# Kernel tuning notes

Measured on AMD Instinct MI355X. Metric: run time of the kernel, lower is better.

## Reference

```python
import jax, jax.numpy as jnp
import numpy as np

B, C, H, W = 64, 1, 256, 256        # x shape; seq_len = C*H = 256, input_dim = W = 256
E, HID, L, NCLS = 512, 1024, 2, 10


def _lstm_layer(xs, h0, c0, Wx, bx, Wh, bh):
    """xs: [S,B,in] -> ys: [S,B,HID]. Gate order: f, i, g(candidate), o."""
    def step(carry, xt):
        h, c = carry
        gates = xt @ Wx + bx + h @ Wh + bh            # [B, 4*HID] (fuses 8 tiny Linears into 2 GEMMs)
        f, i, g, o = jnp.split(gates, 4, axis=-1)
        f = jax.nn.sigmoid(f)
        i = jax.nn.sigmoid(i)
        g = jnp.tanh(g)
        o = jax.nn.sigmoid(o)
        c = f * c + i * g
        h = o * jnp.tanh(c)
        return (h, c), h
    (hT, cT), ys = jax.lax.scan(step, (h0, c0), xs)
    return ys


def setup_inputs() -> dict:
    key = jax.random.key(0)
    ks = jax.random.split(key, 16)
    s = 0.02
    inp = {
        "x": jax.random.normal(ks[0], (B, C, H, W), jnp.float32),
        "h0": jax.random.normal(ks[1], (L, B, HID), jnp.float32),
        "c0": jax.random.normal(ks[2], (L, B, HID), jnp.float32),
        "W_enc": jax.random.normal(ks[3], (W, E), jnp.float32) * s,
        "b_enc": jnp.zeros((E,), jnp.float32),
        "alpha": jnp.float32(0.25),  # PReLU default single-parameter weight
        "Wx0": jax.random.normal(ks[4], (E, 4 * HID), jnp.float32) * s,
        "bx0": jnp.zeros((4 * HID,), jnp.float32),
        "Wh0": jax.random.normal(ks[5], (HID, 4 * HID), jnp.float32) * s,
        "bh0": jnp.zeros((4 * HID,), jnp.float32),
        "Wx1": jax.random.normal(ks[6], (HID, 4 * HID), jnp.float32) * s,
        "bx1": jnp.zeros((4 * HID,), jnp.float32),
        "Wh1": jax.random.normal(ks[7], (HID, 4 * HID), jnp.float32) * s,
        "bh1": jnp.zeros((4 * HID,), jnp.float32),
        "W_cls": jax.random.normal(ks[8], (HID, NCLS), jnp.float32) * s,
        "b_cls": jnp.zeros((NCLS,), jnp.float32),
    }
    return inp


def reference(x, h0, c0, W_enc, b_enc, alpha, Wx0, bx0, Wh0, bh0,
              Wx1, bx1, Wh1, bh1, W_cls, b_cls):
    b, c, h, w = x.shape
    x = x.reshape(b, c * h, w)                    # [B, S, input_dim]
    e = x @ W_enc + b_enc                         # encoder Linear
    e = jnp.where(e >= 0, e, alpha * e)           # PReLU (single shared alpha)
    xs = jnp.swapaxes(e, 0, 1)                    # [S, B, E] for scan
    ys = _lstm_layer(xs, h0[0], c0[0], Wx0, bx0, Wh0, bh0)
    ys = _lstm_layer(ys, h0[1], c0[1], Wx1, bx1, Wh1, bh1)
    return ys[-1] @ W_cls + b_cls                 # classify last timestep -> [B, 10]
```

## Files before the change

kernel.cpp:

```cpp
#include <hip/hip_runtime.h>
#include <hip/hip_bf16.h>
#include <cstddef>


using short8 = __attribute__((ext_vector_type(8))) short;
using f32x4  = __attribute__((ext_vector_type(4))) float;

#define LD8(p) (*reinterpret_cast<const short8*>(p))

__device__ __forceinline__ float sigmoidf_(float x) {
    return 1.f / (1.f + __expf(-x));
}
__device__ __forceinline__ unsigned short f2bf(float x) {
    union { float f; unsigned u; } v; v.f = x;
    unsigned r = v.u + 0x7fffu + ((v.u >> 16) & 1u);
    return (unsigned short)(r >> 16);
}
__device__ __forceinline__ float bf2f(unsigned short h) {
    union { unsigned u; float f; } v; v.u = ((unsigned)h) << 16;
    return v.f;
}

__global__ __launch_bounds__(256) void xsplit_k(
    const float* __restrict__ x, unsigned short* __restrict__ Xhi,
    unsigned short* __restrict__ Xlo)
{
    const int idx = blockIdx.x * 256 + threadIdx.x;
    const int m = idx >> 5, kq = idx & 31;
    const int b = m & 63, t = m >> 6;
    const float* src = x + (size_t)b * 65536 + (size_t)t * 256 + kq * 8;
    short8 hv, lv;
#pragma unroll
    for (int e = 0; e < 8; ++e) {
        const float f = src[e];
        const unsigned short h = f2bf(f);
        hv[e] = (short)h;
        lv[e] = (short)f2bf(f - bf2f(h));
    }
    const size_t o = (size_t)m * 256 + kq * 8;
    *reinterpret_cast<short8*>(Xhi + o) = hv;
    *reinterpret_cast<short8*>(Xlo + o) = lv;
}

__global__ __launch_bounds__(256) void bsplitN_k(
    const float* __restrict__ W, unsigned short* __restrict__ Bhi,
    unsigned short* __restrict__ Blo, int K, int N)
{
    __shared__ float tl[32][65];
    const int k0 = blockIdx.x * 32, n0 = blockIdx.y * 64;
    const int tid = threadIdx.x;
    {
        const int kk = tid >> 3, nq = tid & 7;
#pragma unroll
        for (int j = 0; j < 2; ++j) {
            const float4 v = *reinterpret_cast<const float4*>(
                &W[(size_t)(k0 + kk) * N + n0 + nq * 8 + j * 4]);
            tl[kk][nq * 8 + j * 4 + 0] = v.x; tl[kk][nq * 8 + j * 4 + 1] = v.y;
            tl[kk][nq * 8 + j * 4 + 2] = v.z; tl[kk][nq * 8 + j * 4 + 3] = v.w;
        }
    }
    __syncthreads();
    const int n = tid >> 2, kq = tid & 3;
    short8 hv, lv;
#pragma unroll
    for (int j = 0; j < 8; ++j) {
        const float xv = tl[kq * 8 + j][n];
        const unsigned short h = f2bf(xv);
        hv[j] = (short)h;
        lv[j] = (short)f2bf(xv - bf2f(h));
    }
    const size_t o = (size_t)(n0 + n) * K + k0 + kq * 8;
    *reinterpret_cast<short8*>(&Bhi[o]) = hv;
    *reinterpret_cast<short8*>(&Blo[o]) = lv;
}

__global__ __launch_bounds__(256) void enc_mfma_k(
    const unsigned short* __restrict__ Ahi, const unsigned short* __restrict__ Alo,
    const unsigned short* __restrict__ Bhi, const unsigned short* __restrict__ Blo,
    unsigned short* __restrict__ Ef, const float* __restrict__ benc,
    const float* __restrict__ alphap)
{
    __shared__ float smemf[10240];
    unsigned short* const smemh = (unsigned short*)smemf;
    unsigned short* const As0 = smemh;
    unsigned short* const As1 = smemh + 5120;
    unsigned short* const Bs0 = smemh + 10240;
    unsigned short* const Bs1 = smemh + 15360;

    const int tid = threadIdx.x;
    const int lane = tid & 63, wid = tid >> 6;
    const int wm = wid >> 1, wn = wid & 1;
    const int m0 = blockIdx.y * 128;
    const int n0 = blockIdx.x * 128;
    const int K = 256;

    f32x4 acc[4][4] = {};

    const int sr = tid & 127;
    const int spl = tid >> 7;
    const unsigned short* Ag = (spl ? Alo : Ahi) + (size_t)(m0 + sr) * K;
    const unsigned short* Bg = (spl ? Blo : Bhi) + (size_t)(n0 + sr) * K;
    unsigned short* Asw = (spl ? As1 : As0) + sr * 40;
    unsigned short* Bsw = (spl ? Bs1 : Bs0) + sr * 40;
    const int sw = sr & 3;

    const int kg = lane >> 4;
    const int fr = lane & 15;

    for (int k0 = 0; k0 < K; k0 += 32) {
        short8 av[4], bv[4];
#pragma unroll
        for (int c = 0; c < 4; ++c) {
            av[c] = LD8(Ag + k0 + c * 8);
            bv[c] = LD8(Bg + k0 + c * 8);
        }
        __syncthreads();
#pragma unroll
        for (int c = 0; c < 4; ++c) {
            *reinterpret_cast<short8*>(Asw + ((c ^ sw) * 8)) = av[c];
            *reinterpret_cast<short8*>(Bsw + ((c ^ sw) * 8)) = bv[c];
        }
        __syncthreads();

        short8 af[2][4], bf[2][4];
#pragma unroll
        for (int i = 0; i < 4; ++i) {
            const int ra = wm * 64 + i * 16 + fr;
            const int rb = wn * 64 + i * 16 + fr;
            af[0][i] = LD8(As0 + ra * 40 + ((kg ^ (ra & 3)) * 8));
            af[1][i] = LD8(As1 + ra * 40 + ((kg ^ (ra & 3)) * 8));
            bf[0][i] = LD8(Bs0 + rb * 40 + ((kg ^ (rb & 3)) * 8));
            bf[1][i] = LD8(Bs1 + rb * 40 + ((kg ^ (rb & 3)) * 8));
        }
#pragma unroll
        for (int i = 0; i < 4; ++i)
#pragma unroll
            for (int j = 0; j < 4; ++j) {
                acc[i][j] = __builtin_amdgcn_mfma_f32_16x16x32_bf16(
                    af[0][i], bf[0][j], acc[i][j], 0, 0, 0);
                acc[i][j] = __builtin_amdgcn_mfma_f32_16x16x32_bf16(
                    af[0][i], bf[1][j], acc[i][j], 0, 0, 0);
                acc[i][j] = __builtin_amdgcn_mfma_f32_16x16x32_bf16(
                    af[1][i], bf[0][j], acc[i][j], 0, 0, 0);
            }
    }
    __syncthreads();

    float* slab = smemf + wid * 1040;
    const int t = (m0 >> 6) + wm;
    const int fq = lane >> 4;
    const float alpha = alphap[0];
#pragma unroll 1
    for (int j = 0; j < 4; ++j) {
#pragma unroll
        for (int i = 0; i < 4; ++i)
#pragma unroll
            for (int rr = 0; rr < 4; ++rr)
                slab[fr * 65 + i * 16 + fq * 4 + rr] = acc[i][j][rr];
        __syncthreads();
        const int b = lane;
        const int nj = b >> 4;
#pragma unroll
        for (int ng = 0; ng < 4; ++ng) {
            const int n = n0 + wn * 64 + j * 16 + ng * 4;
            unsigned short hs[4], ls[4];
#pragma unroll
            for (int v = 0; v < 4; ++v) {
                float f = slab[(ng * 4 + v) * 65 + b] + benc[n + v];
                f = (f >= 0.f) ? f : alpha * f;
                hs[v] = f2bf(f);
                ls[v] = f2bf(f - bf2f(hs[v]));
            }
            uint2 hp, lp;
            hp.x = (unsigned)hs[0] | ((unsigned)hs[1] << 16);
            hp.y = (unsigned)hs[2] | ((unsigned)hs[3] << 16);
            lp.x = (unsigned)ls[0] | ((unsigned)ls[1] << 16);
            lp.y = (unsigned)ls[2] | ((unsigned)ls[3] << 16);
            const int s = n >> 5, kgn = (n >> 3) & 3, e0 = n & 7;
            const int ln = (b & 15) + 16 * kgn;
            const size_t base =
                ((((size_t)t * 32 + s) * 4 + nj) * 64 + ln) * 8 + e0;
            *reinterpret_cast<uint2*>(Ef + base) = hp;
            *reinterpret_cast<uint2*>(Ef + base + 32768) = lp;
        }
        __syncthreads();
    }
}

__global__ __launch_bounds__(256) void wprep_k(
    const float* __restrict__ Wa, const float* __restrict__ Wb,
    unsigned short* __restrict__ Wf, int NS)
{
    __shared__ float tl[32][65];
    const int k0 = blockIdx.x * 32, j0 = blockIdx.y * 64;
    const int tid = threadIdx.x;
    {
        const int kk = tid >> 3, jq = tid & 7;
        const int k = k0 + kk;
        const float* src = (k < 1024) ? &Wa[(size_t)k * 4096]
                                      : &Wb[(size_t)(k - 1024) * 4096];
#pragma unroll
        for (int h = 0; h < 2; ++h) {
            const float4 v = *reinterpret_cast<const float4*>(
                &src[j0 + jq * 8 + h * 4]);
            tl[kk][jq * 8 + h * 4 + 0] = v.x; tl[kk][jq * 8 + h * 4 + 1] = v.y;
            tl[kk][jq * 8 + h * 4 + 2] = v.z; tl[kk][jq * 8 + h * 4 + 3] = v.w;
        }
    }
    __syncthreads();
    const int j = tid >> 2, kg = tid & 3;
    const int jg = j0 + j;
    const int g = jg >> 10, cc = jg & 1023;
    const int lb = cc >> 3, c = cc & 7;
    const int rloc = g * 8 + c;
    const int mi = rloc >> 4, r16 = rloc & 15;
    const int lane = r16 + 16 * kg;
    const int s = k0 >> 5;
    short8 hv, lv;
#pragma unroll
    for (int e = 0; e < 8; ++e) {
        const float x = tl[kg * 8 + e][j];
        const unsigned short h = f2bf(x);
        hv[e] = (short)h;
        lv[e] = (short)f2bf(x - bf2f(h));
    }
    const size_t oH = ((((size_t)lb * 2 + 0) * NS + s) * 2 + mi) * 512 + (size_t)lane * 8;
    const size_t oL = ((((size_t)lb * 2 + 1) * NS + s) * 2 + mi) * 512 + (size_t)lane * 8;
    *reinterpret_cast<short8*>(Wf + oH) = hv;
    *reinterpret_cast<short8*>(Wf + oL) = lv;
}

__global__ __launch_bounds__(256) void hsplit_k(
    const float* __restrict__ hrow, unsigned short* __restrict__ dst)
{
    const int idx = blockIdx.x * 256 + threadIdx.x;
    const int b = idx >> 7, gc = idx & 127;
    const int k = gc * 8;
    short8 hv, lv;
#pragma unroll
    for (int e = 0; e < 8; ++e) {
        const float x = hrow[(size_t)b * 1024 + k + e];
        const unsigned short h = f2bf(x);
        hv[e] = (short)h;
        lv[e] = (short)f2bf(x - bf2f(h));
    }
    const int s = k >> 5, kg = (k >> 3) & 3, nj = b >> 4;
    const int l = (b & 15) + 16 * kg;
    const size_t oH = (((size_t)(0 * 32 + s) * 4 + nj) * 64 + l) * 8;
    const size_t oL = (((size_t)(1 * 32 + s) * 4 + nj) * 64 + l) * 8;
    *reinterpret_cast<short8*>(dst + oH) = hv;
    *reinterpret_cast<short8*>(dst + oL) = lv;
}

__global__ __launch_bounds__(256) void bsum_k(
    const float* __restrict__ bx, const float* __restrict__ bh,
    float* __restrict__ out)
{
    const int r = blockIdx.x * 256 + threadIdx.x;
    const int lb = r >> 5, rl = r & 31;
    const int g = rl >> 3, c = rl & 7;
    const int j = g * 1024 + lb * 8 + c;
    out[r] = bx[j] + bh[j];
}

__global__ __launch_bounds__(512, 2) void fused_lstm_k(
    const unsigned short* __restrict__ Ef,
    const unsigned short* __restrict__ Wf0,
    const unsigned short* __restrict__ Wf1,
    unsigned short* __restrict__ Y0, unsigned short* __restrict__ H1,
    const float* __restrict__ c0, const float* __restrict__ bsum0p,
    const float* __restrict__ bsum1p, float* __restrict__ hst1,
    unsigned* bar)
{
    __shared__ float Pred[8][32][66];
    __shared__ unsigned short hasmH[64][8];
    __shared__ unsigned short hasmL[64][8];

    const int tid = threadIdx.x;
    const int lane = tid & 63;
    const int w = tid >> 6;
    const int bid = blockIdx.x;
    const int layer = bid >> 7;
    const int lb = bid & 127;

    const int NS = layer ? 64 : 48;
    const int nEx = layer ? 4 : 2;
    const int wNS = NS * 1024;

    const unsigned short* Wf = layer ? Wf1 : Wf0;
    const unsigned short* wB =
        Wf + (size_t)lb * 2 * NS * 1024 + (size_t)lane * 8;

    short8 w00r[8], w01r[8], w10r[8], w11r[8];
#pragma unroll
    for (int i = 0; i < 8; ++i)
        if (i < 4 + nEx) {
            const int sg = (i < 4)
                ? (w * 4 + i)
                : (layer ? (32 + w * 4 + (i - 4)) : (32 + w * 2 + (i - 4)));
            const unsigned short* wp = wB + (size_t)sg * 1024;
            w00r[i] = LD8(wp);        w01r[i] = LD8(wp + 512);
            w10r[i] = LD8(wp + wNS);  w11r[i] = LD8(wp + wNS + 512);
        }

    const int col = w;
    float c_ = c0[(size_t)layer * 65536 + (size_t)lane * 1024 + lb * 8 + col];
    const float* bsB = layer ? bsum1p : bsum0p;
    float bs[4];
#pragma unroll
    for (int g = 0; g < 4; ++g) bs[g] = bsB[lb * 32 + g * 8 + col];

#define MM(mi, nj, HH, HL)                                                     \
    acc[mi][nj] = __builtin_amdgcn_mfma_f32_16x16x32_bf16(                     \
        (mi) ? w01r[i] : w00r[i], HH, acc[mi][nj], 0, 0, 0);                   \
    acc[mi][nj] = __builtin_amdgcn_mfma_f32_16x16x32_bf16(                     \
        (mi) ? w01r[i] : w00r[i], HL, acc[mi][nj], 0, 0, 0);                   \
    acc[mi][nj] = __builtin_amdgcn_mfma_f32_16x16x32_bf16(                     \
        (mi) ? w11r[i] : w10r[i], HH, acc[mi][nj], 0, 0, 0);
#define SUBTILE(hp, po)                                                        \
    {                                                                          \
        const short8 h0v = LD8(hp),        h1v = LD8(hp + 512);                \
        const short8 h2v = LD8(hp + 1024), h3v = LD8(hp + 1536);               \
        const short8 l0v = LD8(hp + po),        l1v = LD8(hp + po + 512);      \
        const short8 l2v = LD8(hp + po + 1024), l3v = LD8(hp + po + 1536);     \
        MM(0, 0, h0v, l0v)  MM(0, 1, h1v, l1v)                                 \
        MM(0, 2, h2v, l2v)  MM(0, 3, h3v, l3v)                                 \
        MM(1, 0, h0v, l0v)  MM(1, 1, h1v, l1v)                                 \
        MM(1, 2, h2v, l2v)  MM(1, 3, h3v, l3v)                                 \
    }
#define WPOLL(baseIdx, need)                                                   \
    {                                                                          \
        if (lane < 16) {                                                       \
            unsigned* p = bar + (size_t)((baseIdx) + lane) * 32;               \
            while (__hip_atomic_load(p, __ATOMIC_RELAXED,                      \
                                     __HIP_MEMORY_SCOPE_AGENT) < (need))       \
                __builtin_amdgcn_s_sleep(1);                                   \
        }                                                                      \
        __builtin_amdgcn_wave_barrier();                                       \
        asm volatile("" ::: "memory");                                         \
    }

    for (int r = 1; r <= 257; ++r) {
        const bool act = layer ? (r >= 2) : (r <= 256);
        if (act) {
            const int t = layer ? r - 2 : r - 1;
            const unsigned short* hOwn =
                (layer ? H1 : Y0) + (size_t)t * 131072 + (size_t)lane * 8;
            const unsigned short* hCross = layer
                ? Y0 + (size_t)(t + 1) * 131072 + (size_t)lane * 8
                : Ef + (size_t)t * 65536 + (size_t)lane * 8;
            const int poCross = layer ? 65536 : 32768;

            f32x4 acc[2][4] = {};

            if (layer) WPOLL(w * 16, (unsigned)(r - 1))
#pragma unroll
            for (int i = 4; i < 8; ++i)
                if (i < 4 + nEx) {
                    const int cs = layer ? (w * 4 + (i - 4)) : (w * 2 + (i - 4));
                    const unsigned short* hp = hCross + (size_t)cs * 2048;
                    SUBTILE(hp, poCross)
                }

            if (r >= 2) WPOLL((layer ? 128 : 0) + w * 16, (unsigned)(r - 1))
#pragma unroll
            for (int i = 0; i < 4; ++i) {
                const unsigned short* hp = hOwn + (size_t)(w * 4 + i) * 2048;
                SUBTILE(hp, 65536)
            }

            {
                const int rq = (lane >> 4) * 4, cq = lane & 15;
#pragma unroll
                for (int mi = 0; mi < 2; ++mi)
#pragma unroll
                    for (int nj = 0; nj < 4; ++nj)
#pragma unroll
                        for (int rr = 0; rr < 4; ++rr)
                            Pred[w][mi * 16 + rq + rr][nj * 16 + cq] =
                                acc[mi][nj][rr];
            }
            __syncthreads();

            {
                float p[4];
#pragma unroll
                for (int g = 0; g < 4; ++g) {
                    const int row = g * 8 + col;
                    float s0 = 0.f;
#pragma unroll
                    for (int ww = 0; ww < 8; ++ww)
                        s0 += Pred[ww][row][lane];
                    p[g] = s0 + bs[g];
                }
                const float fg = sigmoidf_(p[0]);
                const float ig = sigmoidf_(p[1]);
                const float gg = tanhf(p[2]);
                const float og = sigmoidf_(p[3]);
                c_ = fmaf(fg, c_, ig * gg);
                const float h = og * tanhf(c_);
                const unsigned short hh = f2bf(h);
                hasmH[lane][col] = hh;
                hasmL[lane][col] = f2bf(h - bf2f(hh));
                if (layer && r == 257)
                    hst1[(size_t)(lb * 8 + col) * 64 + lane] = h;
            }
            __syncthreads();

            if (tid < 128) {
                const int p = tid >> 6, b = tid & 63;
                unsigned short* hw =
                    (layer ? H1 : Y0) + (size_t)(t + 1) * 131072;
                const size_t off =
                    (((size_t)(p * 32 + (lb >> 2)) * 4 + (b >> 4)) * 64 +
                     ((b & 15) + 16 * (lb & 3))) * 8;
                const unsigned long long* src =
                    reinterpret_cast<const unsigned long long*>(
                        p ? &hasmL[b][0] : &hasmH[b][0]);
                unsigned long long* dst =
                    reinterpret_cast<unsigned long long*>(hw + off);
                __hip_atomic_store(dst, src[0], __ATOMIC_RELAXED,
                                   __HIP_MEMORY_SCOPE_AGENT);
                __hip_atomic_store(dst + 1, src[1], __ATOMIC_RELAXED,
                                   __HIP_MEMORY_SCOPE_AGENT);
            }
        }

        if (r <= 256) {
            __syncthreads();
            if (tid == 0)
                __hip_atomic_store(bar + (size_t)bid * 32, (unsigned)r,
                                   __ATOMIC_RELAXED, __HIP_MEMORY_SCOPE_AGENT);
        }
    }
#undef WPOLL
#undef SUBTILE
#undef MM
}

__global__ __launch_bounds__(256) void cls_k(
    const float* __restrict__ hfin, const float* __restrict__ Wc,
    const float* __restrict__ bcls, float* __restrict__ out)
{
    __shared__ float red[4][64];
    const int n = blockIdx.x;
    const int lane = threadIdx.x & 63, w = threadIdx.x >> 6;
    float acc = 0.f;
    for (int k = w * 256; k < w * 256 + 256; ++k)
        acc = fmaf(hfin[k * 64 + lane], Wc[k * 10 + n], acc);
    red[w][lane] = acc;
    __syncthreads();
    if (w == 0) {
        out[lane * 10 + n] = red[0][lane] + red[1][lane] + red[2][lane] +
                             red[3][lane] + bcls[n];
    }
}

extern "C" void kernel_launch(void* const* d_in, const int* in_sizes, int n_in,
                              void* d_out, int out_size, void* d_ws,
                              size_t ws_size, hipStream_t stream)
{
    const float* x    = (const float*)d_in[0];
    const float* h0   = (const float*)d_in[1];
    const float* c0   = (const float*)d_in[2];
    const float* Wenc = (const float*)d_in[3];
    const float* benc = (const float*)d_in[4];
    const float* alpha= (const float*)d_in[5];
    const float* Wx0  = (const float*)d_in[6];
    const float* bx0  = (const float*)d_in[7];
    const float* Wh0  = (const float*)d_in[8];
    const float* bh0  = (const float*)d_in[9];
    const float* Wx1  = (const float*)d_in[10];
    const float* bx1  = (const float*)d_in[11];
    const float* Wh1  = (const float*)d_in[12];
    const float* bh1  = (const float*)d_in[13];
    const float* Wcls = (const float*)d_in[14];
    const float* bcls = (const float*)d_in[15];
    float* out = (float*)d_out;

    float* ws = (float*)d_ws;
    size_t off = 0;
    unsigned short* Ef   = (unsigned short*)(ws + off); off += 8388608;
    unsigned short* Wf0  = (unsigned short*)(ws + off); off += 6291456;
    unsigned short* Wf1  = (unsigned short*)(ws + off); off += 8388608;
    unsigned short* Y0   = (unsigned short*)(ws + off); off += 16842752;
    unsigned short* H1   = (unsigned short*)(ws + off); off += 16842752;
    unsigned short* Xhi  = (unsigned short*)(ws + off); off += 2097152;
    unsigned short* Xlo  = (unsigned short*)(ws + off); off += 2097152;
    unsigned short* WeThi= (unsigned short*)(ws + off); off += 65536;
    unsigned short* WeTlo= (unsigned short*)(ws + off); off += 65536;
    float* bsum0p = ws + off; off += 4096;
    float* bsum1p = ws + off; off += 4096;
    float* hst1   = ws + off; off += 65536;
    unsigned* bars = (unsigned*)(ws + off); off += 8192;

    (void)hipMemsetAsync(bars, 0, 32768, stream);

    xsplit_k<<<2048, 256, 0, stream>>>(x, Xhi, Xlo);
    bsplitN_k<<<dim3(8, 8), 256, 0, stream>>>(Wenc, WeThi, WeTlo, 256, 512);
    enc_mfma_k<<<dim3(4, 128), 256, 0, stream>>>(
        Xhi, Xlo, WeThi, WeTlo, Ef, benc, alpha);
    wprep_k<<<dim3(48, 64), 256, 0, stream>>>(Wh0, Wx0, Wf0, 48);
    wprep_k<<<dim3(64, 64), 256, 0, stream>>>(Wh1, Wx1, Wf1, 64);
    hsplit_k<<<32, 256, 0, stream>>>(h0, Y0);
    hsplit_k<<<32, 256, 0, stream>>>(h0 + 65536, H1);
    bsum_k<<<16, 256, 0, stream>>>(bx0, bh0, bsum0p);
    bsum_k<<<16, 256, 0, stream>>>(bx1, bh1, bsum1p);

    fused_lstm_k<<<256, 512, 0, stream>>>(Ef, Wf0, Wf1, Y0, H1, c0,
                                          bsum0p, bsum1p, hst1, bars);

    cls_k<<<dim3(10), 256, 0, stream>>>(hst1, Wcls, bcls, out);
}
```

Before: 1.914 ms.

## Split persistent LSTM across 512 four-column blocks with per-wave barrier signaling

The persistent fused LSTM kernel is repartitioned from 256 blocks of 512 threads, each owning 8 hidden columns, to 512 blocks of 256 threads, each owning 4 columns. Weight prep, bias layout and the h write-out are reworked to match, and each wave now keeps 16 hi/lo weight fragments in registers instead of paired 2-row tiles. The idea is to spread the per-step recurrent GEMM over more CUs so each block does less serial work per timestep. The cost is that every poll now waits on 64 barrier flags instead of 16, which adds more cross-block synchronization traffic. The final block-wide sync before signaling is replaced by a vmcnt wait inside wave 0.

```diff
diff --git a/kernel.cpp b/kernel.cpp
--- a/kernel.cpp
+++ b/kernel.cpp
@@ -187,7 +187,7 @@
     }
 }
 
-__global__ __launch_bounds__(256) void wprep_k(
+__global__ __launch_bounds__(256) void wprep4_k(
     const float* __restrict__ Wa, const float* __restrict__ Wb,
     unsigned short* __restrict__ Wf, int NS)
 {
@@ -211,10 +211,9 @@
     const int j = tid >> 2, kg = tid & 3;
     const int jg = j0 + j;
     const int g = jg >> 10, cc = jg & 1023;
-    const int lb = cc >> 3, c = cc & 7;
-    const int rloc = g * 8 + c;
-    const int mi = rloc >> 4, r16 = rloc & 15;
-    const int lane = r16 + 16 * kg;
+    const int lb = cc >> 2, c = cc & 3;
+    const int rloc = g * 4 + c;
+    const int lane = rloc + 16 * kg;
     const int s = k0 >> 5;
     short8 hv, lv;
 #pragma unroll
@@ -224,8 +223,8 @@
         hv[e] = (short)h;
         lv[e] = (short)f2bf(x - bf2f(h));
     }
-    const size_t oH = ((((size_t)lb * 2 + 0) * NS + s) * 2 + mi) * 512 + (size_t)lane * 8;
-    const size_t oL = ((((size_t)lb * 2 + 1) * NS + s) * 2 + mi) * 512 + (size_t)lane * 8;
+    const size_t oH = (((size_t)lb * 2 + 0) * NS + s) * 512 + (size_t)lane * 8;
+    const size_t oL = (((size_t)lb * 2 + 1) * NS + s) * 512 + (size_t)lane * 8;
     *reinterpret_cast<short8*>(Wf + oH) = hv;
     *reinterpret_cast<short8*>(Wf + oL) = lv;
 }
@@ -252,18 +251,18 @@
     *reinterpret_cast<short8*>(dst + oL) = lv;
 }
 
-__global__ __launch_bounds__(256) void bsum_k(
+__global__ __launch_bounds__(256) void bsum4_k(
     const float* __restrict__ bx, const float* __restrict__ bh,
     float* __restrict__ out)
 {
     const int r = blockIdx.x * 256 + threadIdx.x;
-    const int lb = r >> 5, rl = r & 31;
-    const int g = rl >> 3, c = rl & 7;
-    const int j = g * 1024 + lb * 8 + c;
+    const int lb = r >> 4, rl = r & 15;
+    const int g = rl >> 2, c = rl & 3;
+    const int j = g * 1024 + lb * 4 + c;
     out[r] = bx[j] + bh[j];
 }
 
-__global__ __launch_bounds__(512, 2) void fused_lstm_k(
+__global__ __launch_bounds__(256, 2) void fused_lstm_k(
     const unsigned short* __restrict__ Ef,
     const unsigned short* __restrict__ Wf0,
     const unsigned short* __restrict__ Wf1,
@@ -272,70 +271,60 @@
     const float* __restrict__ bsum1p, float* __restrict__ hst1,
     unsigned* bar)
 {
-    __shared__ float Pred[8][32][66];
-    __shared__ unsigned short hasmH[64][8];
-    __shared__ unsigned short hasmL[64][8];
+    __shared__ float Pred[4][16][66];
+    __shared__ unsigned short hasmH[64][4];
+    __shared__ unsigned short hasmL[64][4];
 
     const int tid = threadIdx.x;
     const int lane = tid & 63;
     const int w = tid >> 6;
     const int bid = blockIdx.x;
-    const int layer = bid >> 7;
-    const int lb = bid & 127;
+    const int layer = bid >> 8;
+    const int lb = bid & 255;
 
     const int NS = layer ? 64 : 48;
-    const int nEx = layer ? 4 : 2;
-    const int wNS = NS * 1024;
+    const int nSub = layer ? 16 : 12;
 
     const unsigned short* Wf = layer ? Wf1 : Wf0;
     const unsigned short* wB =
-        Wf + (size_t)lb * 2 * NS * 1024 + (size_t)lane * 8;
-
-    short8 w00r[8], w01r[8], w10r[8], w11r[8];
-#pragma unroll
-    for (int i = 0; i < 8; ++i)
-        if (i < 4 + nEx) {
-            const int sg = (i < 4)
-                ? (w * 4 + i)
-                : (layer ? (32 + w * 4 + (i - 4)) : (32 + w * 2 + (i - 4)));
-            const unsigned short* wp = wB + (size_t)sg * 1024;
-            w00r[i] = LD8(wp);        w01r[i] = LD8(wp + 512);
-            w10r[i] = LD8(wp + wNS);  w11r[i] = LD8(wp + wNS + 512);
+        Wf + (size_t)lb * 2 * NS * 512 + (size_t)lane * 8;
+
+    short8 wHi[16], wLo[16];
+#pragma unroll
+    for (int i = 0; i < 16; ++i)
+        if (i < nSub) {
+            const int s = (i < 8)
+                ? (w * 8 + i)
+                : (32 + (layer ? w * 8 : w * 4) + (i - 8));
+            wHi[i] = LD8(wB + (size_t)s * 512);
+            wLo[i] = LD8(wB + (size_t)(NS + s) * 512);
         }
 
     const int col = w;
-    float c_ = c0[(size_t)layer * 65536 + (size_t)lane * 1024 + lb * 8 + col];
+    float c_ = c0[(size_t)layer * 65536 + (size_t)lane * 1024 + lb * 4 + col];
     const float* bsB = layer ? bsum1p : bsum0p;
     float bs[4];
 #pragma unroll
-    for (int g = 0; g < 4; ++g) bs[g] = bsB[lb * 32 + g * 8 + col];
-
-#define MM(mi, nj, HH, HL)                                                     \
-    acc[mi][nj] = __builtin_amdgcn_mfma_f32_16x16x32_bf16(                     \
-        (mi) ? w01r[i] : w00r[i], HH, acc[mi][nj], 0, 0, 0);                   \
-    acc[mi][nj] = __builtin_amdgcn_mfma_f32_16x16x32_bf16(                     \
-        (mi) ? w01r[i] : w00r[i], HL, acc[mi][nj], 0, 0, 0);                   \
-    acc[mi][nj] = __builtin_amdgcn_mfma_f32_16x16x32_bf16(                     \
-        (mi) ? w11r[i] : w10r[i], HH, acc[mi][nj], 0, 0, 0);
+    for (int g = 0; g < 4; ++g) bs[g] = bsB[lb * 16 + g * 4 + col];
+
+#define MM(nj, HH, HL)                                                         \
+    acc[nj] = __builtin_amdgcn_mfma_f32_16x16x32_bf16(wHi[i], HH, acc[nj], 0, 0, 0); \
+    acc[nj] = __builtin_amdgcn_mfma_f32_16x16x32_bf16(wHi[i], HL, acc[nj], 0, 0, 0); \
+    acc[nj] = __builtin_amdgcn_mfma_f32_16x16x32_bf16(wLo[i], HH, acc[nj], 0, 0, 0);
 #define SUBTILE(hp, po)                                                        \
     {                                                                          \
         const short8 h0v = LD8(hp),        h1v = LD8(hp + 512);                \
         const short8 h2v = LD8(hp + 1024), h3v = LD8(hp + 1536);               \
         const short8 l0v = LD8(hp + po),        l1v = LD8(hp + po + 512);      \
         const short8 l2v = LD8(hp + po + 1024), l3v = LD8(hp + po + 1536);     \
-        MM(0, 0, h0v, l0v)  MM(0, 1, h1v, l1v)                                 \
-        MM(0, 2, h2v, l2v)  MM(0, 3, h3v, l3v)                                 \
-        MM(1, 0, h0v, l0v)  MM(1, 1, h1v, l1v)                                 \
-        MM(1, 2, h2v, l2v)  MM(1, 3, h3v, l3v)                                 \
+        MM(0, h0v, l0v)  MM(1, h1v, l1v)  MM(2, h2v, l2v)  MM(3, h3v, l3v)     \
     }
 #define WPOLL(baseIdx, need)                                                   \
     {                                                                          \
-        if (lane < 16) {                                                       \
-            unsigned* p = bar + (size_t)((baseIdx) + lane) * 32;               \
-            while (__hip_atomic_load(p, __ATOMIC_RELAXED,                      \
-                                     __HIP_MEMORY_SCOPE_AGENT) < (need))       \
-                __builtin_amdgcn_s_sleep(1);                                   \
-        }                                                                      \
+        unsigned* p = bar + (size_t)((baseIdx) + lane) * 32;                   \
+        while (__hip_atomic_load(p, __ATOMIC_RELAXED,                          \
+                                 __HIP_MEMORY_SCOPE_AGENT) < (need))           \
+            __builtin_amdgcn_s_sleep(1);                                       \
         __builtin_amdgcn_wave_barrier();                                       \
         asm volatile("" ::: "memory");                                         \
     }
@@ -351,34 +340,31 @@
                 : Ef + (size_t)t * 65536 + (size_t)lane * 8;
             const int poCross = layer ? 65536 : 32768;
 
-            f32x4 acc[2][4] = {};
-
-            if (layer) WPOLL(w * 16, (unsigned)(r - 1))
-#pragma unroll
-            for (int i = 4; i < 8; ++i)
-                if (i < 4 + nEx) {
-                    const int cs = layer ? (w * 4 + (i - 4)) : (w * 2 + (i - 4));
+            f32x4 acc[4] = {};
+
+            if (layer) WPOLL(w * 64, (unsigned)(r - 1))
+#pragma unroll
+            for (int i = 8; i < 16; ++i)
+                if (i < nSub) {
+                    const int cs = (layer ? w * 8 : w * 4) + (i - 8);
                     const unsigned short* hp = hCross + (size_t)cs * 2048;
                     SUBTILE(hp, poCross)
                 }
 
-            if (r >= 2) WPOLL((layer ? 128 : 0) + w * 16, (unsigned)(r - 1))
-#pragma unroll
-            for (int i = 0; i < 4; ++i) {
-                const unsigned short* hp = hOwn + (size_t)(w * 4 + i) * 2048;
+            if (r >= 2) WPOLL((layer ? 256 : 0) + w * 64, (unsigned)(r - 1))
+#pragma unroll
+            for (int i = 0; i < 8; ++i) {
+                const unsigned short* hp = hOwn + (size_t)(w * 8 + i) * 2048;
                 SUBTILE(hp, 65536)
             }
 
             {
                 const int rq = (lane >> 4) * 4, cq = lane & 15;
 #pragma unroll
-                for (int mi = 0; mi < 2; ++mi)
-#pragma unroll
-                    for (int nj = 0; nj < 4; ++nj)
-#pragma unroll
-                        for (int rr = 0; rr < 4; ++rr)
-                            Pred[w][mi * 16 + rq + rr][nj * 16 + cq] =
-                                acc[mi][nj][rr];
+                for (int nj = 0; nj < 4; ++nj)
+#pragma unroll
+                    for (int rr = 0; rr < 4; ++rr)
+                        Pred[w][rq + rr][nj * 16 + cq] = acc[nj][rr];
             }
             __syncthreads();
 
@@ -386,12 +372,9 @@
                 float p[4];
 #pragma unroll
                 for (int g = 0; g < 4; ++g) {
-                    const int row = g * 8 + col;
-                    float s0 = 0.f;
-#pragma unroll
-                    for (int ww = 0; ww < 8; ++ww)
-                        s0 += Pred[ww][row][lane];
-                    p[g] = s0 + bs[g];
+                    const int row = g * 4 + col;
+                    p[g] = Pred[0][row][lane] + Pred[1][row][lane] +
+                           Pred[2][row][lane] + Pred[3][row][lane] + bs[g];
                 }
                 const float fg = sigmoidf_(p[0]);
                 const float ig = sigmoidf_(p[1]);
@@ -403,32 +386,38 @@
                 hasmH[lane][col] = hh;
                 hasmL[lane][col] = f2bf(h - bf2f(hh));
                 if (layer && r == 257)
-                    hst1[(size_t)(lb * 8 + col) * 64 + lane] = h;
+                    hst1[(size_t)(lb * 4 + col) * 64 + lane] = h;
             }
             __syncthreads();
 
-            if (tid < 128) {
-                const int p = tid >> 6, b = tid & 63;
+            if (w == 0) {
                 unsigned short* hw =
                     (layer ? H1 : Y0) + (size_t)(t + 1) * 131072;
-                const size_t off =
-                    (((size_t)(p * 32 + (lb >> 2)) * 4 + (b >> 4)) * 64 +
-                     ((b & 15) + 16 * (lb & 3))) * 8;
-                const unsigned long long* src =
-                    reinterpret_cast<const unsigned long long*>(
-                        p ? &hasmL[b][0] : &hasmH[b][0]);
-                unsigned long long* dst =
-                    reinterpret_cast<unsigned long long*>(hw + off);
-                __hip_atomic_store(dst, src[0], __ATOMIC_RELAXED,
-                                   __HIP_MEMORY_SCOPE_AGENT);
-                __hip_atomic_store(dst + 1, src[1], __ATOMIC_RELAXED,
-                                   __HIP_MEMORY_SCOPE_AGENT);
+                const int s = lb >> 3, kg2 = (lb >> 1) & 3;
+                const int e0 = (lb & 1) * 4;
+                const int b = lane;
+                const size_t offH =
+                    (((size_t)s * 4 + (b >> 4)) * 64 +
+                     ((b & 15) + 16 * kg2)) * 8 + e0;
+                __hip_atomic_store(
+                    reinterpret_cast<unsigned long long*>(hw + offH),
+                    *reinterpret_cast<const unsigned long long*>(&hasmH[b][0]),
+                    __ATOMIC_RELAXED, __HIP_MEMORY_SCOPE_AGENT);
+                __hip_atomic_store(
+                    reinterpret_cast<unsigned long long*>(hw + offH + 65536),
+                    *reinterpret_cast<const unsigned long long*>(&hasmL[b][0]),
+                    __ATOMIC_RELAXED, __HIP_MEMORY_SCOPE_AGENT);
+                if (r <= 256) {
+                    asm volatile("s_waitcnt vmcnt(0)" ::: "memory");
+                    __builtin_amdgcn_wave_barrier();
+                    if (lane == 0)
+                        __hip_atomic_store(bar + (size_t)bid * 32, (unsigned)r,
+                                           __ATOMIC_RELAXED,
+                                           __HIP_MEMORY_SCOPE_AGENT);
+                }
             }
-        }
-
-        if (r <= 256) {
-            __syncthreads();
-            if (tid == 0)
+        } else {
+            if (r <= 256 && tid == 0)
                 __hip_atomic_store(bar + (size_t)bid * 32, (unsigned)r,
                                    __ATOMIC_RELAXED, __HIP_MEMORY_SCOPE_AGENT);
         }
@@ -492,22 +481,22 @@
     float* bsum0p = ws + off; off += 4096;
     float* bsum1p = ws + off; off += 4096;
     float* hst1   = ws + off; off += 65536;
-    unsigned* bars = (unsigned*)(ws + off); off += 8192;
-
-    (void)hipMemsetAsync(bars, 0, 32768, stream);
+    unsigned* bars = (unsigned*)(ws + off); off += 16384;
+
+    (void)hipMemsetAsync(bars, 0, 65536, stream);
 
     xsplit_k<<<2048, 256, 0, stream>>>(x, Xhi, Xlo);
     bsplitN_k<<<dim3(8, 8), 256, 0, stream>>>(Wenc, WeThi, WeTlo, 256, 512);
     enc_mfma_k<<<dim3(4, 128), 256, 0, stream>>>(
         Xhi, Xlo, WeThi, WeTlo, Ef, benc, alpha);
-    wprep_k<<<dim3(48, 64), 256, 0, stream>>>(Wh0, Wx0, Wf0, 48);
-    wprep_k<<<dim3(64, 64), 256, 0, stream>>>(Wh1, Wx1, Wf1, 64);
+    wprep4_k<<<dim3(48, 64), 256, 0, stream>>>(Wh0, Wx0, Wf0, 48);
+    wprep4_k<<<dim3(64, 64), 256, 0, stream>>>(Wh1, Wx1, Wf1, 64);
     hsplit_k<<<32, 256, 0, stream>>>(h0, Y0);
     hsplit_k<<<32, 256, 0, stream>>>(h0 + 65536, H1);
-    bsum_k<<<16, 256, 0, stream>>>(bx0, bh0, bsum0p);
-    bsum_k<<<16, 256, 0, stream>>>(bx1, bh1, bsum1p);
-
-    fused_lstm_k<<<256, 512, 0, stream>>>(Ef, Wf0, Wf1, Y0, H1, c0,
+    bsum4_k<<<16, 256, 0, stream>>>(bx0, bh0, bsum0p);
+    bsum4_k<<<16, 256, 0, stream>>>(bx1, bh1, bsum1p);
+
+    fused_lstm_k<<<512, 256, 0, stream>>>(Ef, Wf0, Wf1, Y0, H1, c0,
                                           bsum0p, bsum1p, hst1, bars);
 
     cls_k<<<dim3(10), 256, 0, stream>>>(hst1, Wcls, bcls, out);
```

Result: slower. 3.999 ms (+108.9%).
